# Kernel tuning notes

Measured on AMD Instinct MI355X. Metric: run time of the kernel, lower is better.

The kernel has to match this reference:

```python
import jax, jax.numpy as jnp
import numpy as np
import math

B, S, D_IN, EMBED, H = 4, 1024, 1024, 1024, 16
HD = EMBED // H  # 64


def setup_inputs() -> dict:
    key = jax.random.key(0)
    ks = jax.random.split(key, 8)
    x = jax.random.normal(ks[0], (B, S, D_IN), dtype=jnp.float32)
    mask = jax.random.randint(ks[1], (B, S, S), 0, 2, dtype=jnp.int32)
    weights = jax.random.uniform(ks[2], (B, S, S), dtype=jnp.float32)
    # xavier-uniform-ish scale for projections
    lim_qkv = math.sqrt(6.0 / (D_IN + 3 * EMBED))
    lim_o = math.sqrt(6.0 / (EMBED + EMBED))
    W_qkv = jax.random.uniform(ks[3], (3 * EMBED, D_IN), minval=-lim_qkv, maxval=lim_qkv, dtype=jnp.float32)
    b_qkv = jnp.zeros((3 * EMBED,), dtype=jnp.float32)
    W_o = jax.random.uniform(ks[4], (EMBED, EMBED), minval=-lim_o, maxval=lim_o, dtype=jnp.float32)
    b_o = jnp.zeros((EMBED,), dtype=jnp.float32)
    return {"x": x, "mask": mask, "weights": weights, "W_qkv": W_qkv, "b_qkv": b_qkv, "W_o": W_o, "b_o": b_o}


def reference(x, mask, weights, W_qkv, b_qkv, W_o, b_o):
    b, s, _ = x.shape
    # QKV projection: [b, s, 3*EMBED] -> [b, H, s, 3*HD]
    qkv = (x @ W_qkv.T + b_qkv).reshape(b, s, H, 3 * HD).transpose(0, 2, 1, 3)
    q, k, v = jnp.split(qkv, 3, axis=-1)  # each [b, H, s, HD]
    logits = jnp.einsum('bhqd,bhkd->bhqk', q, k) / math.sqrt(HD)
    logits = jnp.where(mask[:, None, :, :] == 0, jnp.float32(-9e15), logits)
    # weights transposed on last two dims, broadcast over heads
    w = jnp.swapaxes(weights, -2, -1)[:, None, :, :]  # [b, 1, s, s]
    m = jnp.max(logits, axis=-1, keepdims=True)
    e = w * jnp.exp(logits - m)
    attn = e / jnp.sum(e, axis=-1, keepdims=True)
    vals = jnp.einsum('bhqk,bhkd->bhqd', attn, v)
    vals = vals.transpose(0, 2, 1, 3).reshape(b, s, EMBED)
    return vals @ W_o.T + b_o
```

## Files before the change

kernel.cpp:

```cpp
#include <hip/hip_runtime.h>
#include <hip/hip_bf16.h>
#include <stdint.h>

#define SDIM 1024
#define BATCH 4
#define NH 16
#define HDIM 64
#define KDIM 1024
#define N_QKV 3072
#define EMB 1024

typedef uint16_t u16;
typedef __attribute__((ext_vector_type(4))) float f32x4;
typedef __attribute__((ext_vector_type(8))) short bf16x8;
typedef __attribute__((ext_vector_type(8))) unsigned short u16x8;

__device__ __forceinline__ u16 f2bf(float f) {
  union { float f; uint32_t u; } x; x.f = f;
  uint32_t r = x.u + 0x7FFFu + ((x.u >> 16) & 1u);
  return (u16)(r >> 16);
}

__device__ __forceinline__ float bf2f(u16 b) {
  union { uint32_t u; float f; } x; x.u = ((uint32_t)b) << 16;
  return x.f;
}

__device__ __forceinline__ void gload_lds16(const u16* g, u16* l) {
  __builtin_amdgcn_global_load_lds(
      (const __attribute__((address_space(1))) unsigned int*)g,
      (__attribute__((address_space(3))) unsigned int*)l, 16, 0, 0);
}

#define N8_X  524288
#define N8_WQ 393216
#define N8_WO 131072
#define NCVT  1048576
#define NWM3  262144
__global__ void prep_kernel(const float* __restrict__ a, const float* __restrict__ bq,
                            const float* __restrict__ co,
                            u16* __restrict__ oa, u16* __restrict__ ob, u16* __restrict__ oc,
                            const int* __restrict__ mask, const float* __restrict__ wts,
                            u16* __restrict__ wm3) {
  const int total = NCVT + NWM3;
  const size_t SS = (size_t)SDIM * SDIM;
  int stride = gridDim.x * blockDim.x;
  for (int i = blockIdx.x * blockDim.x + threadIdx.x; i < total; i += stride) {
    if (i < NCVT) {
      const float* s; u16* d; int j;
      if (i < N8_X)             { s = a;  d = oa; j = i; }
      else if (i < N8_X + N8_WQ){ s = bq; d = ob; j = i - N8_X; }
      else                      { s = co; d = oc; j = i - N8_X - N8_WQ; }
      const float4* s4 = (const float4*)s + (size_t)j * 2;
      float4 u = s4[0], v = s4[1];
      u16x8 o;
      o[0] = f2bf(u.x); o[1] = f2bf(u.y); o[2] = f2bf(u.z); o[3] = f2bf(u.w);
      o[4] = f2bf(v.x); o[5] = f2bf(v.y); o[6] = f2bf(v.z); o[7] = f2bf(v.w);
      ((u16x8*)d)[j] = o;
    } else {
      int t = i - NCVT;
      int lane = t & 63, kt = (t >> 6) & 15, T = (t >> 10) & 63, b = t >> 16;
      int g2 = lane >> 4, c2 = lane & 15;
      int q = T * 16 + c2;
      const int* mrow = mask + (size_t)b * SS + (size_t)q * SDIM;
      const float* wcol = wts + (size_t)b * SS + q;
      u16* dst = wm3 + ((size_t)(b * 64 + T) * 16 + kt) * 1024 + lane * 16;
      #pragma unroll
      for (int hf = 0; hf < 2; ++hf) {
        int bk = kt * 64 + 8 * g2 + 32 * hf;
        int4 m0 = *(const int4*)(mrow + bk);
        int4 m1 = *(const int4*)(mrow + bk + 4);
        int mm[8] = {m0.x, m0.y, m0.z, m0.w, m1.x, m1.y, m1.z, m1.w};
        u16x8 o;
        #pragma unroll
        for (int e = 0; e < 8; ++e)
          o[e] = mm[e] ? f2bf(wcol[(size_t)(bk + e) * SDIM]) : (u16)0;
        *(u16x8*)(dst + hf * 8) = o;
      }
    }
  }
}

__global__ __launch_bounds__(512, 1) void gemm_qkv(
    const u16* __restrict__ A, const u16* __restrict__ Bm,
    const float* __restrict__ bias,
    u16* __restrict__ Qh, u16* __restrict__ Kh, u16* __restrict__ Vt)
{
  __shared__ char smem[114688];
  const int tid = threadIdx.x;
  const int gid = blockIdx.x;
  const int brow = (gid & 15) * 256, bcol = (gid >> 4) * 192;
  const int wid = tid >> 6, lane = tid & 63;
  const int g = lane >> 4, c = lane & 15, cx = c & 7;
  const int wr = wid & 3, wc = wid >> 2;

  const u16* asrc[4]; int adoff[4];
  #pragma unroll
  for (int j = 0; j < 4; ++j) {
    int i = j * 512 + tid;
    int row = i >> 3, sch = (i & 7) ^ (row & 7);
    asrc[j] = A + (size_t)(brow + row) * KDIM + sch * 8;
    adoff[j] = (j * 512 + wid * 64) * 16;
  }
  const u16* bsrc[3]; int bdoff[3];
  #pragma unroll
  for (int j = 0; j < 3; ++j) {
    int i = j * 512 + tid;
    int row = i >> 3, sch = (i & 7) ^ (row & 7);
    bsrc[j] = Bm + (size_t)(bcol + row) * KDIM + sch * 8;
    bdoff[j] = 32768 + (j * 512 + wid * 64) * 16;
  }

  auto stage = [&](int kt, int slot) {
    char* base = smem + slot * 57344;
    #pragma unroll
    for (int j = 0; j < 4; ++j)
      gload_lds16(asrc[j] + kt * 64, (u16*)(base + adoff[j]));
    #pragma unroll
    for (int j = 0; j < 3; ++j)
      gload_lds16(bsrc[j] + kt * 64, (u16*)(base + bdoff[j]));
  };

  f32x4 acc[4][6] = {};

  stage(0, 0);
  __syncthreads();

  for (int kt = 0; kt < 16; ++kt) {
    if (kt < 15) stage(kt + 1, (kt + 1) & 1);

    const char* As = smem + (kt & 1) * 57344;
    const char* Bs = As + 32768;

    #pragma unroll
    for (int kk = 0; kk < 2; ++kk) {
      bf16x8 af[4], bfr[6];
      #pragma unroll
      for (int m = 0; m < 4; ++m) {
        int row = wr * 64 + m * 16 + c;
        af[m] = *(const bf16x8*)(As + (row << 7) + ((((kk << 2) + g) ^ cx) << 4));
      }
      #pragma unroll
      for (int n = 0; n < 6; ++n) {
        int row = wc * 96 + n * 16 + c;
        bfr[n] = *(const bf16x8*)(Bs + (row << 7) + ((((kk << 2) + g) ^ cx) << 4));
      }
      __builtin_amdgcn_s_setprio(1);
      #pragma unroll
      for (int m = 0; m < 4; ++m)
        #pragma unroll
        for (int n = 0; n < 6; ++n)
          acc[m][n] = __builtin_amdgcn_mfma_f32_16x16x32_bf16(
              af[m], bfr[n], acc[m][n], 0, 0, 0);
      __builtin_amdgcn_s_setprio(0);
    }
    __syncthreads();
  }

  #pragma unroll
  for (int m = 0; m < 4; ++m) {
    #pragma unroll
    for (int n = 0; n < 6; ++n) {
      int col = bcol + wc * 96 + n * 16 + c;
      float bv = bias[col];
      int h = col / 192;
      int rem = col - h * 192;
      int sec = rem >> 6, d = rem & 63;
      #pragma unroll
      for (int r = 0; r < 4; ++r) {
        int row = brow + wr * 64 + m * 16 + g * 4 + r;
        int b = row >> 10, sl = row & 1023;
        float v = acc[m][n][r] + bv;
        if (sec == 0)
          Qh[((size_t)(b * NH + h) * SDIM + sl) * HDIM + d] = f2bf(v * 0.18033688f);
        else if (sec == 1)
          Kh[((size_t)(b * NH + h) * SDIM + sl) * HDIM + d] = f2bf(v);
        else
          Vt[((size_t)(b * NH + h) * HDIM + d) * SDIM + sl] = f2bf(v);
      }
    }
  }
}

__global__ __launch_bounds__(256) void gemm_bt(
    const u16* __restrict__ A, const u16* __restrict__ Bm,
    const float* __restrict__ bias, float* __restrict__ C,
    int M, int N, int K)
{
  __shared__ u16 As[128 * 64];
  __shared__ u16 Bs[128 * 64];
  const int tid = threadIdx.x;
  const int wid = tid >> 6, lane = tid & 63;
  const int g = lane >> 4, c = lane & 15, cx = c & 7;
  const int wrow = (wid >> 1) * 64, wcol = (wid & 1) * 64;
  const int brow = blockIdx.x * 128, bcol = blockIdx.y * 128;

  const u16* asrc[4]; const u16* bsrc[4]; u16* adst[4]; u16* bdst[4];
  #pragma unroll
  for (int j = 0; j < 4; ++j) {
    int ci = j * 256 + tid;
    int row = ci >> 3, sch = (ci & 7) ^ (row & 7);
    asrc[j] = A  + (size_t)(brow + row) * K + sch * 8;
    bsrc[j] = Bm + (size_t)(bcol + row) * K + sch * 8;
    adst[j] = As + (j * 256 + wid * 64) * 8;
    bdst[j] = Bs + (j * 256 + wid * 64) * 8;
  }

  f32x4 acc[4][4] = {};
  const char* Asc = (const char*)As;
  const char* Bsc = (const char*)Bs;

  for (int kt = 0; kt < K / 64; ++kt) {
    #pragma unroll
    for (int j = 0; j < 4; ++j) {
      gload_lds16(asrc[j] + kt * 64, adst[j]);
      gload_lds16(bsrc[j] + kt * 64, bdst[j]);
    }
    __syncthreads();

    bf16x8 af[2][4], bfr[2][4];
    #pragma unroll
    for (int kk = 0; kk < 2; ++kk)
      #pragma unroll
      for (int i = 0; i < 4; ++i) {
        int cha = ((kk << 2) + g) ^ cx;
        af[kk][i]  = *(const bf16x8*)(Asc + ((wrow + i * 16 + c) << 7) + (cha << 4));
        bfr[kk][i] = *(const bf16x8*)(Bsc + ((wcol + i * 16 + c) << 7) + (cha << 4));
      }
    #pragma unroll
    for (int kk = 0; kk < 2; ++kk)
      #pragma unroll
      for (int mi = 0; mi < 4; ++mi)
        #pragma unroll
        for (int ni = 0; ni < 4; ++ni)
          acc[mi][ni] = __builtin_amdgcn_mfma_f32_16x16x32_bf16(
              af[kk][mi], bfr[kk][ni], acc[mi][ni], 0, 0, 0);
    __syncthreads();
  }

  #pragma unroll
  for (int mi = 0; mi < 4; ++mi)
    #pragma unroll
    for (int ni = 0; ni < 4; ++ni) {
      int col = bcol + wcol + ni * 16 + c;
      float bv = bias[col];
      #pragma unroll
      for (int r = 0; r < 4; ++r) {
        int row = brow + wrow + mi * 16 + g * 4 + r;
        C[(size_t)row * N + col] = acc[mi][ni][r] + bv;
      }
    }
}

__global__ __launch_bounds__(256, 4) void attn_kernel(
    const u16* __restrict__ Qh, const u16* __restrict__ Kh, const u16* __restrict__ Vt,
    const u16* __restrict__ wm3, u16* __restrict__ vals)
{
  int bid = blockIdx.x;
  int swz = (bid & 7) * 128 + (bid >> 3);
  const int qt = swz & 15, bh = swz >> 4;
  const int h = bh & 15, b = bh >> 4;

  const int tid = threadIdx.x;
  const int wid = tid >> 6, lane = tid & 63;
  const int g = lane >> 4, c = lane & 15;
  const int qloc = qt * 64 + wid * 16;

  __shared__ u16 Kb[2][4096];
  __shared__ u16 Vb[2][4096];

  const u16* qp = Qh + ((size_t)bh * SDIM + qloc + c) * HDIM;
  bf16x8 qa0 = *(const bf16x8*)(qp + g * 8);
  bf16x8 qa1 = *(const bf16x8*)(qp + 32 + g * 8);

  const u16* kbase = Kh + (size_t)bh * SDIM * HDIM;
  const u16* vbase = Vt + (size_t)bh * HDIM * SDIM;
  const u16* wbase = wm3 + (((size_t)(b * 16 + qt) * 4 + wid) * 16) * 1024 + lane * 16;

  float l_run = 0.f;
  f32x4 acc_o[4] = {};

  auto fsw = [](int row) { return ((row ^ (row >> 3)) & 7) ^ ((row & 1) << 2); };

  int kro[4], kxr[4], vro[4], vxr[4];
  #pragma unroll
  for (int st = 0; st < 4; ++st) {
    int kr = ((c >> 2) << 3) + ((st & 1) << 2) + (c & 3) + ((st >> 1) << 5);
    kro[st] = kr << 7;
    kxr[st] = fsw(kr);
  }
  #pragma unroll
  for (int dt = 0; dt < 4; ++dt) {
    int vr = dt * 16 + c;
    vro[dt] = vr << 7;
    vxr[dt] = fsw(vr);
  }

  auto stage = [&](int buf, int kt) {
    const int k0 = kt * 64;
    #pragma unroll
    for (int j = 0; j < 2; ++j) {
      int i = j * 256 + tid;
      int row = i >> 3;
      int sch = (i & 7) ^ (((row ^ (row >> 3)) & 7) ^ ((row & 1) << 2));
      gload_lds16(kbase + (size_t)(k0 + row) * HDIM + sch * 8,
                  &Kb[buf][(size_t)(j * 256 + wid * 64) * 8]);
      gload_lds16(vbase + (size_t)row * SDIM + k0 + sch * 8,
                  &Vb[buf][(size_t)(j * 256 + wid * 64) * 8]);
    }
  };

  stage(0, 0);
  __syncthreads();
  int cur = 0;

  for (int kt = 0; kt < 16; ++kt) {
    if (kt < 15) stage(cur ^ 1, kt + 1);

    u16x8 w0 = *(const u16x8*)(wbase + kt * 1024);
    u16x8 w1 = *(const u16x8*)(wbase + kt * 1024 + 8);

    const char* kb = (const char*)&Kb[cur][0];
    const char* vb = (const char*)&Vb[cur][0];

    f32x4 sc[4];
    #pragma unroll
    for (int st = 0; st < 4; ++st) {
      bf16x8 ka0 = *(const bf16x8*)(kb + kro[st] + ((g ^ kxr[st]) << 4));
      bf16x8 ka1 = *(const bf16x8*)(kb + kro[st] + (((4 + g) ^ kxr[st]) << 4));
      f32x4 z = {};
      z = __builtin_amdgcn_mfma_f32_16x16x32_bf16(ka0, qa0, z, 0, 0, 0);
      z = __builtin_amdgcn_mfma_f32_16x16x32_bf16(ka1, qa1, z, 0, 0, 0);
      sc[st] = z;
    }

    float p[4][4];
    #pragma unroll
    for (int st = 0; st < 4; ++st) {
      #pragma unroll
      for (int r = 0; r < 4; ++r) {
        u16 wv = (st < 2) ? ((const u16*)&w0)[st * 4 + r]
                          : ((const u16*)&w1)[(st - 2) * 4 + r];
        float pv = bf2f(wv) * __builtin_amdgcn_exp2f(sc[st][r]);
        p[st][r] = pv;
        l_run += pv;
      }
    }

    uint32_t pk[8];
    #pragma unroll
    for (int i = 0; i < 8; ++i) {
      float lo = p[i >> 1][(i & 1) * 2], hi = p[i >> 1][(i & 1) * 2 + 1];
      asm("v_cvt_pk_bf16_f32 %0, %1, %2" : "=v"(pk[i]) : "v"(lo), "v"(hi));
    }
    union PA { uint32_t u[4]; bf16x8 v; } a0, a1;
    #pragma unroll
    for (int i = 0; i < 4; ++i) { a0.u[i] = pk[i]; a1.u[i] = pk[4 + i]; }

    #pragma unroll
    for (int dt = 0; dt < 4; ++dt) {
      bf16x8 vb0 = *(const bf16x8*)(vb + vro[dt] + ((g ^ vxr[dt]) << 4));
      bf16x8 vb1 = *(const bf16x8*)(vb + vro[dt] + (((4 + g) ^ vxr[dt]) << 4));
      acc_o[dt] = __builtin_amdgcn_mfma_f32_16x16x32_bf16(a0.v, vb0, acc_o[dt], 0, 0, 0);
      acc_o[dt] = __builtin_amdgcn_mfma_f32_16x16x32_bf16(a1.v, vb1, acc_o[dt], 0, 0, 0);
    }

    __syncthreads();
    cur ^= 1;
  }

  l_run += __shfl_xor(l_run, 16);
  l_run += __shfl_xor(l_run, 32);

  float inv[4];
  #pragma unroll
  for (int r = 0; r < 4; ++r)
    inv[r] = 1.0f / __shfl(l_run, g * 4 + r);

  #pragma unroll
  for (int dt = 0; dt < 4; ++dt)
    #pragma unroll
    for (int r = 0; r < 4; ++r) {
      int row = b * SDIM + qloc + g * 4 + r;
      vals[(size_t)row * EMB + h * HDIM + dt * 16 + c] = f2bf(acc_o[dt][r] * inv[r]);
    }
}

extern "C" void kernel_launch(void* const* d_in, const int* in_sizes, int n_in,
                              void* d_out, int out_size, void* d_ws, size_t ws_size,
                              hipStream_t stream) {
  const float* x     = (const float*)d_in[0];
  const int*   mask  = (const int*)d_in[1];
  const float* wts   = (const float*)d_in[2];
  const float* W_qkv = (const float*)d_in[3];
  const float* b_qkv = (const float*)d_in[4];
  const float* W_o   = (const float*)d_in[5];
  const float* b_o   = (const float*)d_in[6];
  float* out = (float*)d_out;

  char* ws = (char*)d_ws;
  u16* xb   = (u16*)(ws);
  u16* wqb  = (u16*)(ws + (8ull  << 20));
  u16* wob  = (u16*)(ws + (14ull << 20));
  u16* Qh   = (u16*)(ws + (16ull << 20));
  u16* Kh   = (u16*)(ws + (24ull << 20));
  u16* Vt   = (u16*)(ws + (32ull << 20));
  u16* valb = (u16*)(ws + (40ull << 20));
  u16* wm3b = (u16*)d_out;

  prep_kernel<<<2048, 256, 0, stream>>>(x, W_qkv, W_o, xb, wqb, wob, mask, wts, wm3b);

  gemm_qkv<<<256, 512, 0, stream>>>(xb, wqb, b_qkv, Qh, Kh, Vt);

  attn_kernel<<<1024, 256, 0, stream>>>(Qh, Kh, Vt, wm3b, valb);

  dim3 g3(32, 8);
  gemm_bt<<<g3, 256, 0, stream>>>(valb, wob, b_o, out, BATCH * SDIM, EMB, KDIM);
}
```

Before: 107.7 us.

## Retile QKV GEMM to 128x128 blocks with swizzled grid, drop double buffering

Replaces the 256x192 double-buffered QKV GEMM (512 threads, one block per CU, 112KB LDS) with a 128x128 single-buffered tile over 768 blocks of 256 threads, plus a block-index swizzle for L2 locality. The goal is higher occupancy and better load balance across CUs, since 256 blocks underfill the device. In exchange, each tile has lower arithmetic intensity and loads are no longer overlapped with MFMA work within a block, so the kernel depends on multiple resident blocks to hide memory latency.

```diff
diff --git a/kernel.cpp b/kernel.cpp
--- a/kernel.cpp
+++ b/kernel.cpp
@@ -81,96 +81,79 @@
   }
 }
 
-__global__ __launch_bounds__(512, 1) void gemm_qkv(
+__global__ __launch_bounds__(256) void gemm_qkv(
     const u16* __restrict__ A, const u16* __restrict__ Bm,
     const float* __restrict__ bias,
     u16* __restrict__ Qh, u16* __restrict__ Kh, u16* __restrict__ Vt)
 {
-  __shared__ char smem[114688];
+  __shared__ u16 As[128 * 64];
+  __shared__ u16 Bs[128 * 64];
   const int tid = threadIdx.x;
-  const int gid = blockIdx.x;
-  const int brow = (gid & 15) * 256, bcol = (gid >> 4) * 192;
+  int bid = blockIdx.x;
+  int swz = (bid & 7) * 96 + (bid >> 3);
+  const int brow = (swz & 31) << 7, bcol = (swz >> 5) << 7;
   const int wid = tid >> 6, lane = tid & 63;
   const int g = lane >> 4, c = lane & 15, cx = c & 7;
-  const int wr = wid & 3, wc = wid >> 2;
-
-  const u16* asrc[4]; int adoff[4];
+  const int wrow = (wid >> 1) * 64, wcol = (wid & 1) * 64;
+  const int K = KDIM;
+
+  const u16* asrc[4]; const u16* bsrc[4]; u16* adst[4]; u16* bdst[4];
   #pragma unroll
   for (int j = 0; j < 4; ++j) {
-    int i = j * 512 + tid;
-    int row = i >> 3, sch = (i & 7) ^ (row & 7);
-    asrc[j] = A + (size_t)(brow + row) * KDIM + sch * 8;
-    adoff[j] = (j * 512 + wid * 64) * 16;
-  }
-  const u16* bsrc[3]; int bdoff[3];
-  #pragma unroll
-  for (int j = 0; j < 3; ++j) {
-    int i = j * 512 + tid;
-    int row = i >> 3, sch = (i & 7) ^ (row & 7);
-    bsrc[j] = Bm + (size_t)(bcol + row) * KDIM + sch * 8;
-    bdoff[j] = 32768 + (j * 512 + wid * 64) * 16;
-  }
-
-  auto stage = [&](int kt, int slot) {
-    char* base = smem + slot * 57344;
-    #pragma unroll
-    for (int j = 0; j < 4; ++j)
-      gload_lds16(asrc[j] + kt * 64, (u16*)(base + adoff[j]));
-    #pragma unroll
-    for (int j = 0; j < 3; ++j)
-      gload_lds16(bsrc[j] + kt * 64, (u16*)(base + bdoff[j]));
-  };
-
-  f32x4 acc[4][6] = {};
-
-  stage(0, 0);
-  __syncthreads();
-
-  for (int kt = 0; kt < 16; ++kt) {
-    if (kt < 15) stage(kt + 1, (kt + 1) & 1);
-
-    const char* As = smem + (kt & 1) * 57344;
-    const char* Bs = As + 32768;
-
-    #pragma unroll
-    for (int kk = 0; kk < 2; ++kk) {
-      bf16x8 af[4], bfr[6];
-      #pragma unroll
-      for (int m = 0; m < 4; ++m) {
-        int row = wr * 64 + m * 16 + c;
-        af[m] = *(const bf16x8*)(As + (row << 7) + ((((kk << 2) + g) ^ cx) << 4));
-      }
-      #pragma unroll
-      for (int n = 0; n < 6; ++n) {
-        int row = wc * 96 + n * 16 + c;
-        bfr[n] = *(const bf16x8*)(Bs + (row << 7) + ((((kk << 2) + g) ^ cx) << 4));
-      }
-      __builtin_amdgcn_s_setprio(1);
-      #pragma unroll
-      for (int m = 0; m < 4; ++m)
+    int ci = j * 256 + tid;
+    int row = ci >> 3, sch = (ci & 7) ^ (row & 7);
+    asrc[j] = A  + (size_t)(brow + row) * K + sch * 8;
+    bsrc[j] = Bm + (size_t)(bcol + row) * K + sch * 8;
+    adst[j] = As + (j * 256 + wid * 64) * 8;
+    bdst[j] = Bs + (j * 256 + wid * 64) * 8;
+  }
+
+  f32x4 acc[4][4] = {};
+  const char* Asc = (const char*)As;
+  const char* Bsc = (const char*)Bs;
+
+  for (int kt = 0; kt < K / 64; ++kt) {
+    #pragma unroll
+    for (int j = 0; j < 4; ++j) {
+      gload_lds16(asrc[j] + kt * 64, adst[j]);
+      gload_lds16(bsrc[j] + kt * 64, bdst[j]);
+    }
+    __syncthreads();
+
+    bf16x8 af[2][4], bfr[2][4];
+    #pragma unroll
+    for (int kk = 0; kk < 2; ++kk)
+      #pragma unroll
+      for (int i = 0; i < 4; ++i) {
+        int cha = ((kk << 2) + g) ^ cx;
+        af[kk][i]  = *(const bf16x8*)(Asc + ((wrow + i * 16 + c) << 7) + (cha << 4));
+        bfr[kk][i] = *(const bf16x8*)(Bsc + ((wcol + i * 16 + c) << 7) + (cha << 4));
+      }
+    #pragma unroll
+    for (int kk = 0; kk < 2; ++kk)
+      #pragma unroll
+      for (int mi = 0; mi < 4; ++mi)
         #pragma unroll
-        for (int n = 0; n < 6; ++n)
-          acc[m][n] = __builtin_amdgcn_mfma_f32_16x16x32_bf16(
-              af[m], bfr[n], acc[m][n], 0, 0, 0);
-      __builtin_amdgcn_s_setprio(0);
-    }
+        for (int ni = 0; ni < 4; ++ni)
+          acc[mi][ni] = __builtin_amdgcn_mfma_f32_16x16x32_bf16(
+              af[kk][mi], bfr[kk][ni], acc[mi][ni], 0, 0, 0);
     __syncthreads();
   }
 
   #pragma unroll
-  for (int m = 0; m < 4; ++m) {
-    #pragma unroll
-    for (int n = 0; n < 6; ++n) {
-      int col = bcol + wc * 96 + n * 16 + c;
+  for (int mi = 0; mi < 4; ++mi) {
+    #pragma unroll
+    for (int ni = 0; ni < 4; ++ni) {
+      int col = bcol + wcol + ni * 16 + c;
       float bv = bias[col];
       int h = col / 192;
       int rem = col - h * 192;
       int sec = rem >> 6, d = rem & 63;
       #pragma unroll
       for (int r = 0; r < 4; ++r) {
-        int row = brow + wr * 64 + m * 16 + g * 4 + r;
+        int row = brow + wrow + mi * 16 + g * 4 + r;
         int b = row >> 10, sl = row & 1023;
-        float v = acc[m][n][r] + bv;
+        float v = acc[mi][ni][r] + bv;
         if (sec == 0)
           Qh[((size_t)(b * NH + h) * SDIM + sl) * HDIM + d] = f2bf(v * 0.18033688f);
         else if (sec == 1)
@@ -410,7 +393,7 @@
 
   prep_kernel<<<2048, 256, 0, stream>>>(x, W_qkv, W_o, xb, wqb, wob, mask, wts, wm3b);
 
-  gemm_qkv<<<256, 512, 0, stream>>>(xb, wqb, b_qkv, Qh, Kh, Vt);
+  gemm_qkv<<<768, 256, 0, stream>>>(xb, wqb, b_qkv, Qh, Kh, Vt);
 
   attn_kernel<<<1024, 256, 0, stream>>>(Qh, Kh, Vt, wm3b, valb);
 
```

Result: slower. 126.2 us (+17.2%).
